# Performance work log

Measured on AMD Instinct MI355X. Metric: run time of the kernel, lower is better.

The kernel has to match this reference:

```python
import jax, jax.numpy as jnp
import numpy as np

N = 50000   # nodes
E = 800000  # edges (avg degree 16)
D = 128     # in_features == out_features (residual)
NEG_SLOPE = 0.2
BN_EPS = 1e-5


def setup_inputs() -> dict:
    key = jax.random.key(0)
    ks = jax.random.split(key, 8)
    x = jax.random.normal(ks[0], (N, D), jnp.float32)
    edge_index = jax.random.randint(ks[1], (2, E), 0, N, dtype=jnp.int32)
    W = jax.random.normal(ks[2], (D, D), jnp.float32) * 0.05
    att_src = jax.random.normal(ks[3], (D,), jnp.float32) * 0.1
    att_dst = jax.random.normal(ks[4], (D,), jnp.float32) * 0.1
    bias = jax.random.normal(ks[5], (D,), jnp.float32) * 0.01
    gamma = jnp.ones((D,), jnp.float32) + jax.random.normal(ks[6], (D,), jnp.float32) * 0.05
    beta = jax.random.normal(ks[7], (D,), jnp.float32) * 0.05
    return {"x": x, "edge_index": edge_index, "W": W, "att_src": att_src,
            "att_dst": att_dst, "bias": bias, "gamma": gamma, "beta": beta}


def reference(x, edge_index, W, att_src, att_dst, bias, gamma, beta):
    src, dst = edge_index[0], edge_index[1]
    # Linear transform (GATConv lin)
    h = x @ W                                   # [N, D]
    # Per-node attention logit halves
    a_s = h @ att_src                           # [N]
    a_d = h @ att_dst                           # [N]
    # Per-edge logits + LeakyReLU
    e = jax.nn.leaky_relu(a_s[src] + a_d[dst], NEG_SLOPE)  # [E]
    # Segment softmax over destination neighborhoods
    m = jax.ops.segment_max(e, dst, num_segments=N)        # [N]
    m = jnp.where(jnp.isfinite(m), m, 0.0)
    p = jnp.exp(e - m[dst])                                 # [E]
    denom = jax.ops.segment_sum(p, dst, num_segments=N)    # [N]
    alpha = p / denom[dst]                                  # [E]
    # Scatter-aggregate weighted neighbor features
    y = jax.ops.segment_sum(alpha[:, None] * h[src], dst, num_segments=N)  # [N, D]
    y = y + bias
    # NormDropRes (eval mode): BN with running_mean=0, running_var=1; dropout off
    yn = gamma * (y / jnp.sqrt(1.0 + BN_EPS)) + beta
    yn = jax.nn.relu(yn)
    # residual: in==out so base = x
    return x + yn
```

## Files before the change

### kernel.cpp

```cpp
#include <hip/hip_runtime.h>
#include <math.h>

#define NN 50000
#define EE 800000
#define DD 128
#define NEG 0.2f
#define SLOT 48

typedef short bf16x8 __attribute__((ext_vector_type(8)));
typedef float f32x4  __attribute__((ext_vector_type(4)));
typedef int   i32x4  __attribute__((ext_vector_type(4)));

__device__ __forceinline__ unsigned short f2bf(float f) {
    unsigned u = __float_as_uint(f);
    unsigned r = u + 0x7fffu + ((u >> 16) & 1u);
    return (unsigned short)(r >> 16);
}

__global__ void k_init(const float* __restrict__ W, unsigned short* __restrict__ wt,
                       int* __restrict__ cursor)
{
    int idx = blockIdx.x * blockDim.x + threadIdx.x;
    if (idx < DD * DD) {
        int k = idx >> 7, n = idx & 127;
        wt[n * DD + k] = f2bf(W[idx]);
    }
    if (idx < NN) cursor[idx] = 0;
}

#define XS_STRIDE 136
__global__ __launch_bounds__(256) void k_fused(
        const float* __restrict__ x, const unsigned short* __restrict__ wtg,
        const float* __restrict__ att_src, const float* __restrict__ att_dst,
        unsigned short* __restrict__ hb, float* __restrict__ a_s, float* __restrict__ a_d,
        const int* __restrict__ ei, int* __restrict__ cursor,
        unsigned short* __restrict__ slots)
{
    __shared__ short xs[64 * XS_STRIDE];
    __shared__ short ws[DD * XS_STRIDE];

    const int t = threadIdx.x;

    if (blockIdx.x & 1) {
        int idx = (int)(blockIdx.x >> 1) * 256 + t;
        if (idx < EE / 4) {
            const i32x4 s4 = __builtin_nontemporal_load(&((const i32x4*)ei)[idx]);
            const i32x4 d4 = __builtin_nontemporal_load(&((const i32x4*)(ei + EE))[idx]);
            int p0 = atomicAdd(&cursor[d4.x], 1);
            int p1 = atomicAdd(&cursor[d4.y], 1);
            int p2 = atomicAdd(&cursor[d4.z], 1);
            int p3 = atomicAdd(&cursor[d4.w], 1);
            if (p0 < SLOT) __builtin_nontemporal_store((unsigned short)s4.x, &slots[d4.x * SLOT + p0]);
            if (p1 < SLOT) __builtin_nontemporal_store((unsigned short)s4.y, &slots[d4.y * SLOT + p1]);
            if (p2 < SLOT) __builtin_nontemporal_store((unsigned short)s4.z, &slots[d4.z * SLOT + p2]);
            if (p3 < SLOT) __builtin_nontemporal_store((unsigned short)s4.w, &slots[d4.w * SLOT + p3]);
        }
        return;
    }

    const int row0 = (int)(blockIdx.x >> 1) * 64;

#pragma unroll
    for (int i = 0; i < 4; i++) {
        int idx = t + i * 256;
        int m = idx >> 4, c = idx & 15;
        int row = row0 + m;
        float4 f0 = make_float4(0.f, 0.f, 0.f, 0.f), f1 = f0;
        if (row < NN) {
            const float* p = x + (size_t)row * DD + c * 8;
            f0 = *(const float4*)p;
            f1 = *(const float4*)(p + 4);
        }
        bf16x8 v;
        v[0] = (short)f2bf(f0.x); v[1] = (short)f2bf(f0.y);
        v[2] = (short)f2bf(f0.z); v[3] = (short)f2bf(f0.w);
        v[4] = (short)f2bf(f1.x); v[5] = (short)f2bf(f1.y);
        v[6] = (short)f2bf(f1.z); v[7] = (short)f2bf(f1.w);
        *(bf16x8*)&xs[m * XS_STRIDE + c * 8] = v;
    }
#pragma unroll
    for (int i = 0; i < 8; i++) {
        int idx = t + i * 256;
        int n = idx >> 4, c = idx & 15;
        uint4 v = ((const uint4*)wtg)[idx];
        *(uint4*)&ws[n * XS_STRIDE + c * 8] = v;
    }
    __syncthreads();

    const int wv = t >> 6;
    const int lane = t & 63;
    const int n0 = lane & 15;
    const int quad = lane >> 4;

    bf16x8 afr[4];
#pragma unroll
    for (int kc = 0; kc < 4; kc++)
        afr[kc] = *(const bf16x8*)&xs[(wv * 16 + n0) * XS_STRIDE + kc * 32 + quad * 8];

    f32x4 acc[8];
#pragma unroll
    for (int nt = 0; nt < 8; nt++) {
        f32x4 a = {0.f, 0.f, 0.f, 0.f};
#pragma unroll
        for (int kc = 0; kc < 4; kc++) {
            bf16x8 bfr = *(const bf16x8*)&ws[(nt * 16 + n0) * XS_STRIDE + kc * 32 + quad * 8];
            a = __builtin_amdgcn_mfma_f32_16x16x32_bf16(afr[kc], bfr, a, 0, 0, 0);
        }
        acc[nt] = a;
    }

    const int rbase = row0 + wv * 16 + quad * 4;
    float ss[4] = {0.f, 0.f, 0.f, 0.f};
    float sd[4] = {0.f, 0.f, 0.f, 0.f};
#pragma unroll
    for (int nt = 0; nt < 8; nt++) {
        int col = nt * 16 + n0;
        float asc = att_src[col], adc = att_dst[col];
#pragma unroll
        for (int r = 0; r < 4; r++) {
            float v = acc[nt][r];
            ss[r] = fmaf(v, asc, ss[r]);
            sd[r] = fmaf(v, adc, sd[r]);
            int row = rbase + r;
            if (row < NN) hb[(size_t)row * DD + col] = f2bf(v);
        }
    }
#pragma unroll
    for (int r = 0; r < 4; r++) {
#pragma unroll
        for (int off = 1; off < 16; off <<= 1) {
            ss[r] += __shfl_xor(ss[r], off);
            sd[r] += __shfl_xor(sd[r], off);
        }
    }
    if (n0 == 0) {
#pragma unroll
        for (int r = 0; r < 4; r++) {
            int row = rbase + r;
            if (row < NN) { a_s[row] = ss[r]; a_d[row] = sd[r]; }
        }
    }
}

__global__ __launch_bounds__(256) void k_node(
        const int* __restrict__ cursor, const unsigned short* __restrict__ slots,
        const float* __restrict__ a_s, const float* __restrict__ a_d,
        const unsigned short* __restrict__ hb, const float* __restrict__ x,
        const float* __restrict__ bias, const float* __restrict__ gamma,
        const float* __restrict__ beta, float* __restrict__ out)
{
    int node = (int)((blockIdx.x * blockDim.x + threadIdx.x) >> 6);
    int lane = threadIdx.x & 63;
    if (node >= NN) return;

    int deg = cursor[node];
    deg = deg > SLOT ? SLOT : deg;
    float ad = a_d[node];

    int s = 0;
    float p = 0.f;
    if (lane < deg) {
        s = (int)slots[node * SLOT + lane];
        float e = a_s[s] + ad;
        e = e > 0.f ? e : NEG * e;
        p = __expf(e);
    }
    float l = p;
#pragma unroll
    for (int off = 32; off > 0; off >>= 1)
        l += __shfl_xor(l, off);

    const int eq = lane >> 4;
    const int fl = lane & 15;
    float acc[8];
#pragma unroll
    for (int k = 0; k < 8; k++) acc[k] = 0.f;

    for (int t = 0; t < deg; t += 8) {
        int i0 = t + eq, i1 = t + 4 + eq;
        int   st0 = __shfl(s, i0);
        int   st1 = __shfl(s, i1);
        float pt0 = __shfl(p, i0);
        float pt1 = __shfl(p, i1);
        uint4 hv0 = *(const uint4*)(hb + ((size_t)st0 << 7) + fl * 8);
        uint4 hv1 = *(const uint4*)(hb + ((size_t)st1 << 7) + fl * 8);
        acc[0] = fmaf(pt0, __uint_as_float(hv0.x << 16),          acc[0]);
        acc[1] = fmaf(pt0, __uint_as_float(hv0.x & 0xffff0000u),  acc[1]);
        acc[2] = fmaf(pt0, __uint_as_float(hv0.y << 16),          acc[2]);
        acc[3] = fmaf(pt0, __uint_as_float(hv0.y & 0xffff0000u),  acc[3]);
        acc[4] = fmaf(pt0, __uint_as_float(hv0.z << 16),          acc[4]);
        acc[5] = fmaf(pt0, __uint_as_float(hv0.z & 0xffff0000u),  acc[5]);
        acc[6] = fmaf(pt0, __uint_as_float(hv0.w << 16),          acc[6]);
        acc[7] = fmaf(pt0, __uint_as_float(hv0.w & 0xffff0000u),  acc[7]);
        acc[0] = fmaf(pt1, __uint_as_float(hv1.x << 16),          acc[0]);
        acc[1] = fmaf(pt1, __uint_as_float(hv1.x & 0xffff0000u),  acc[1]);
        acc[2] = fmaf(pt1, __uint_as_float(hv1.y << 16),          acc[2]);
        acc[3] = fmaf(pt1, __uint_as_float(hv1.y & 0xffff0000u),  acc[3]);
        acc[4] = fmaf(pt1, __uint_as_float(hv1.z << 16),          acc[4]);
        acc[5] = fmaf(pt1, __uint_as_float(hv1.z & 0xffff0000u),  acc[5]);
        acc[6] = fmaf(pt1, __uint_as_float(hv1.w << 16),          acc[6]);
        acc[7] = fmaf(pt1, __uint_as_float(hv1.w & 0xffff0000u),  acc[7]);
    }

#pragma unroll
    for (int off = 16; off < 64; off <<= 1) {
#pragma unroll
        for (int k = 0; k < 8; k++)
            acc[k] += __shfl_xor(acc[k], off);
    }

    if (eq == 0) {
        float invl = (deg > 0) ? 1.f / l : 0.f;
        const float invbn = 0.9999950000374997f;
        int c0 = fl * 8;
        const float* bp = bias  + c0;
        const float* gp = gamma + c0;
        const float* ep = beta  + c0;
        const float* xp = x + ((size_t)node << 7) + c0;
        float* op = out + ((size_t)node << 7) + c0;
        float4 o0, o1;
        float* oo[2] = {(float*)&o0, (float*)&o1};
#pragma unroll
        for (int k = 0; k < 8; k++) {
            float y  = acc[k] * invl + bp[k];
            float yn = gp[k] * (y * invbn) + ep[k];
            yn = yn > 0.f ? yn : 0.f;
            oo[k >> 2][k & 3] = xp[k] + yn;
        }
        *(float4*)op       = o0;
        *(float4*)(op + 4) = o1;
    }
}

extern "C" void kernel_launch(void* const* d_in, const int* in_sizes, int n_in,
                              void* d_out, int out_size, void* d_ws, size_t ws_size,
                              hipStream_t stream)
{
    const float* x     = (const float*)d_in[0];
    const int*   ei    = (const int*)  d_in[1];
    const float* W     = (const float*)d_in[2];
    const float* att_s = (const float*)d_in[3];
    const float* att_d = (const float*)d_in[4];
    const float* bias  = (const float*)d_in[5];
    const float* gamma = (const float*)d_in[6];
    const float* beta  = (const float*)d_in[7];
    float* out = (float*)d_out;

    int*            cursor = (int*)d_ws;
    unsigned short* slots  = (unsigned short*)(cursor + NN);
    float*          a_sv   = (float*)(slots + (size_t)NN * SLOT);
    float*          a_dv   = a_sv + NN;
    unsigned short* wtg    = (unsigned short*)(a_dv + NN);
    unsigned short* hb     = wtg + DD * DD;

    const int gemm_blocks = (NN + 63) / 64;
    k_init <<<(NN + 255) / 256, 256, 0, stream>>>(W, wtg, cursor);
    k_fused<<<2 * gemm_blocks, 256, 0, stream>>>(x, wtg, att_s, att_d, hb,
                                                 a_sv, a_dv, ei, cursor, slots);
    k_node <<<(NN * 64 + 255) / 256, 256, 0, stream>>>(cursor, slots, a_sv, a_dv,
                                                        hb, x, bias, gamma, beta, out);
}
```

Before: 169.6 us.

## Pre-bucket edges by destination range before scattering into adjacency slots

Adds a pass in k_init that partitions edges into 8 buckets by destination-node range, using shared-memory counters and one global atomic per bucket per block, and writes (src,dst) pairs into per-bucket regions. The scatter blocks in k_fused then read the bucketed pairs, so cursor atomics and slot stores from concurrently running blocks hit a narrower destination range and should get better L2 locality. This costs an extra write and read of 6.4 MB of pair data, a memset launch, and an enlarged grid whose surplus GEMM blocks exit early. It also assumes no bucket holds more than CAP edges.

```diff
diff --git a/kernel.cpp b/kernel.cpp
--- a/kernel.cpp
+++ b/kernel.cpp
@@ -6,6 +6,9 @@
 #define DD 128
 #define NEG 0.2f
 #define SLOT 48
+#define NB 8
+#define BDIV 6250
+#define CAP 102400
 
 typedef short bf16x8 __attribute__((ext_vector_type(8)));
 typedef float f32x4  __attribute__((ext_vector_type(4)));
@@ -17,15 +20,46 @@
     return (unsigned short)(r >> 16);
 }
 
-__global__ void k_init(const float* __restrict__ W, unsigned short* __restrict__ wt,
-                       int* __restrict__ cursor)
+__global__ __launch_bounds__(256) void k_init(
+        const float* __restrict__ W, unsigned short* __restrict__ wt,
+        int* __restrict__ cursor, const int* __restrict__ ei,
+        int* __restrict__ bucket_cnt, int2* __restrict__ pairs)
 {
-    int idx = blockIdx.x * blockDim.x + threadIdx.x;
-    if (idx < DD * DD) {
+    const int t = threadIdx.x;
+    if (blockIdx.x < 64) {
+        int idx = blockIdx.x * 256 + t;
         int k = idx >> 7, n = idx & 127;
         wt[n * DD + k] = f2bf(W[idx]);
-    }
-    if (idx < NN) cursor[idx] = 0;
+        for (int i = idx; i < NN; i += 16384) cursor[i] = 0;
+        return;
+    }
+
+    __shared__ int lcnt[NB];
+    __shared__ int lbase[NB];
+    if (t < NB) lcnt[t] = 0;
+    __syncthreads();
+
+    int idx = (int)(blockIdx.x - 64) * 256 + t;
+    i32x4 s4 = {0,0,0,0}, d4 = {0,0,0,0};
+    int b[4], lp[4];
+    bool valid = idx < EE / 4;
+    if (valid) {
+        s4 = __builtin_nontemporal_load(&((const i32x4*)ei)[idx]);
+        d4 = __builtin_nontemporal_load(&((const i32x4*)(ei + EE))[idx]);
+        b[0] = d4.x / BDIV; lp[0] = atomicAdd(&lcnt[b[0]], 1);
+        b[1] = d4.y / BDIV; lp[1] = atomicAdd(&lcnt[b[1]], 1);
+        b[2] = d4.z / BDIV; lp[2] = atomicAdd(&lcnt[b[2]], 1);
+        b[3] = d4.w / BDIV; lp[3] = atomicAdd(&lcnt[b[3]], 1);
+    }
+    __syncthreads();
+    if (t < NB) lbase[t] = atomicAdd(&bucket_cnt[t], lcnt[t]);
+    __syncthreads();
+    if (valid) {
+        pairs[b[0] * CAP + lbase[b[0]] + lp[0]] = make_int2(s4.x, d4.x);
+        pairs[b[1] * CAP + lbase[b[1]] + lp[1]] = make_int2(s4.y, d4.y);
+        pairs[b[2] * CAP + lbase[b[2]] + lp[2]] = make_int2(s4.z, d4.z);
+        pairs[b[3] * CAP + lbase[b[3]] + lp[3]] = make_int2(s4.w, d4.w);
+    }
 }
 
 #define XS_STRIDE 136
@@ -33,8 +67,8 @@
         const float* __restrict__ x, const unsigned short* __restrict__ wtg,
         const float* __restrict__ att_src, const float* __restrict__ att_dst,
         unsigned short* __restrict__ hb, float* __restrict__ a_s, float* __restrict__ a_d,
-        const int* __restrict__ ei, int* __restrict__ cursor,
-        unsigned short* __restrict__ slots)
+        const int* __restrict__ bucket_cnt, const int2* __restrict__ pairs,
+        int* __restrict__ cursor, unsigned short* __restrict__ slots)
 {
     __shared__ short xs[64 * XS_STRIDE];
     __shared__ short ws[DD * XS_STRIDE];
@@ -42,23 +76,24 @@
     const int t = threadIdx.x;
 
     if (blockIdx.x & 1) {
-        int idx = (int)(blockIdx.x >> 1) * 256 + t;
-        if (idx < EE / 4) {
-            const i32x4 s4 = __builtin_nontemporal_load(&((const i32x4*)ei)[idx]);
-            const i32x4 d4 = __builtin_nontemporal_load(&((const i32x4*)(ei + EE))[idx]);
-            int p0 = atomicAdd(&cursor[d4.x], 1);
-            int p1 = atomicAdd(&cursor[d4.y], 1);
-            int p2 = atomicAdd(&cursor[d4.z], 1);
-            int p3 = atomicAdd(&cursor[d4.w], 1);
-            if (p0 < SLOT) __builtin_nontemporal_store((unsigned short)s4.x, &slots[d4.x * SLOT + p0]);
-            if (p1 < SLOT) __builtin_nontemporal_store((unsigned short)s4.y, &slots[d4.y * SLOT + p1]);
-            if (p2 < SLOT) __builtin_nontemporal_store((unsigned short)s4.z, &slots[d4.z * SLOT + p2]);
-            if (p3 < SLOT) __builtin_nontemporal_store((unsigned short)s4.w, &slots[d4.w * SLOT + p3]);
+        int base = (int)(blockIdx.x >> 1) * 1024;
+#pragma unroll
+        for (int k = 0; k < 4; k++) {
+            int g = base + t + k * 256;
+            int b = g / CAP;
+            int j = g - b * CAP;
+            if (j < bucket_cnt[b]) {
+                int2 pr = pairs[(size_t)b * CAP + j];
+                int pos = atomicAdd(&cursor[pr.y], 1);
+                if (pos < SLOT) slots[pr.y * SLOT + pos] = (unsigned short)pr.x;
+            }
         }
         return;
     }
 
-    const int row0 = (int)(blockIdx.x >> 1) * 64;
+    const int g = (int)(blockIdx.x >> 1);
+    if (g >= (NN + 63) / 64) return;
+    const int row0 = g * 64;
 
 #pragma unroll
     for (int i = 0; i < 4; i++) {
@@ -246,17 +281,22 @@
     const float* beta  = (const float*)d_in[7];
     float* out = (float*)d_out;
 
-    int*            cursor = (int*)d_ws;
-    unsigned short* slots  = (unsigned short*)(cursor + NN);
-    float*          a_sv   = (float*)(slots + (size_t)NN * SLOT);
-    float*          a_dv   = a_sv + NN;
-    unsigned short* wtg    = (unsigned short*)(a_dv + NN);
-    unsigned short* hb     = wtg + DD * DD;
-
-    const int gemm_blocks = (NN + 63) / 64;
-    k_init <<<(NN + 255) / 256, 256, 0, stream>>>(W, wtg, cursor);
-    k_fused<<<2 * gemm_blocks, 256, 0, stream>>>(x, wtg, att_s, att_d, hb,
-                                                 a_sv, a_dv, ei, cursor, slots);
+    int*            cursor     = (int*)d_ws;
+    int*            bucket_cnt = cursor + NN;
+    int2*           pairs      = (int2*)(bucket_cnt + NB);
+    unsigned short* slots      = (unsigned short*)(pairs + (size_t)NB * CAP);
+    float*          a_sv       = (float*)(slots + (size_t)NN * SLOT);
+    float*          a_dv       = a_sv + NN;
+    unsigned short* wtg        = (unsigned short*)(a_dv + NN);
+    unsigned short* hb         = wtg + DD * DD;
+
+    hipMemsetAsync(bucket_cnt, 0, NB * sizeof(int), stream);
+
+    k_init <<<64 + (EE / 4 + 255) / 256, 256, 0, stream>>>(W, wtg, cursor, ei,
+                                                           bucket_cnt, pairs);
+    k_fused<<<2 * (NB * CAP / 1024), 256, 0, stream>>>(x, wtg, att_s, att_d, hb,
+                                                       a_sv, a_dv, bucket_cnt,
+                                                       pairs, cursor, slots);
     k_node <<<(NN * 64 + 255) / 256, 256, 0, stream>>>(cursor, slots, a_sv, a_dv,
                                                         hb, x, bias, gamma, beta, out);
 }
```

Result: slower. 193.2 us (+13.9%).
